# Kernel optimization log

Measured on AMD Instinct MI355X. Metric: run time of the kernel, lower is better.

The kernel has to match this reference:

```python
import jax, jax.numpy as jnp
import numpy as np

N_NODES = 50000
N_EDGES = 800000
IN_CH = 256
OUT_CH = 64  # heads=1
NEG_SLOPE = 0.2


def setup_inputs() -> dict:
    key = jax.random.key(0)
    k1, k2, k3, k4, k5 = jax.random.split(key, 5)
    x = jax.random.normal(k1, (N_NODES, IN_CH), dtype=jnp.float32)
    edge_index = jax.random.randint(k2, (2, N_EDGES), 0, N_NODES, dtype=jnp.int64)
    # glorot init for dense weight [out, in] (torch Linear layout) and att [out, 2]
    s_w = np.sqrt(6.0 / (OUT_CH + IN_CH)).astype(np.float32)
    W = jax.random.uniform(k3, (OUT_CH, IN_CH), minval=-s_w, maxval=s_w, dtype=jnp.float32)
    b = jnp.zeros((OUT_CH,), dtype=jnp.float32)
    s_a = np.sqrt(6.0 / (OUT_CH + 2)).astype(np.float32)
    att = jax.random.uniform(k4, (OUT_CH, 2), minval=-s_a, maxval=s_a, dtype=jnp.float32)
    return {"x": x, "edge_index": edge_index, "W": W, "b": b, "att": att}


def reference(x, edge_index, W, b, att):
    n = x.shape[0]
    # dense projection: feature [N, OUT_CH]
    feature = x @ W.T + b
    # per-node attention contributions: e_pre [N, 2]
    e_pre = feature @ att
    tar = edge_index[0]  # flow='target_to_source'
    src = edge_index[1]
    # edge logit = leakyrelu(a_tar(t) + a_src(s)); self-loop logit per node
    logit_edge = jax.nn.leaky_relu(e_pre[tar, 0] + e_pre[src, 1], NEG_SLOPE)
    logit_self = jax.nn.leaky_relu(e_pre[:, 0] + e_pre[:, 1], NEG_SLOPE)
    # segment softmax over {self edge} U {incoming edges} per target node
    m = jnp.maximum(jax.ops.segment_max(logit_edge, tar, num_segments=n), logit_self)
    exp_edge = jnp.exp(logit_edge - m[tar])
    exp_self = jnp.exp(logit_self - m)
    denom = exp_self + jax.ops.segment_sum(exp_edge, tar, num_segments=n)
    alpha = exp_edge / denom[tar]          # [E]
    alpha_self = exp_self / denom          # [N]
    # weighted gather-scatter aggregation (fused_gas_agg)
    msgs = alpha[:, None] * feature[src]   # [E, OUT_CH]
    out = alpha_self[:, None] * feature + jax.ops.segment_sum(msgs, tar, num_segments=n)
    return out
```

## Files before the change

### kernel.cpp

```cpp
#include <hip/hip_runtime.h>
#include <math.h>

#define N_NODES 50000
#define N_EDGES 800000
#define IN_CH 256
#define OUT_CH 64
#define NEG_SLOPE 0.2f

#define SCAN_BLK 256
#define N_SCAN_BLKS ((N_NODES + SCAN_BLK - 1) / SCAN_BLK)

typedef __bf16 bf16x4 __attribute__((ext_vector_type(4)));
typedef __bf16 bf16x8 __attribute__((ext_vector_type(8)));
typedef float  f32x4  __attribute__((ext_vector_type(4)));

__global__ __launch_bounds__(256) void k_gemm(
    const float* __restrict__ x, const float* __restrict__ W,
    const float* __restrict__ bias, const float* __restrict__ att,
    float* __restrict__ feature, float* __restrict__ e0,
    float* __restrict__ e1, int* __restrict__ deg)
{
    __shared__ __bf16 Ah[64][72];
    __shared__ __bf16 Al[64][72];
    __shared__ __bf16 Bh[64][72];
    __shared__ __bf16 Bl[64][72];

    const int t    = threadIdx.x;
    const int row0 = blockIdx.x * 64;
    const int wv   = t >> 6;
    const int li   = t & 63;
    const int lm   = li & 15;
    const int lq   = li >> 4;

    if (t < 64 && row0 + t < N_NODES) deg[row0 + t] = 0;

    f32x4 acc[4];
    #pragma unroll
    for (int tn = 0; tn < 4; ++tn) acc[tn] = (f32x4){0.f, 0.f, 0.f, 0.f};

    const int sr = t >> 2;
    const int cq = t & 3;

    for (int kc = 0; kc < IN_CH; kc += 64) {
        __syncthreads();
        {
            int gr = row0 + sr;
            #pragma unroll
            for (int i = 0; i < 4; ++i) {
                float4 v = make_float4(0.f, 0.f, 0.f, 0.f);
                if (gr < N_NODES)
                    v = *reinterpret_cast<const float4*>(&x[(size_t)gr * IN_CH + kc + cq * 16 + i * 4]);
                __bf16 hx = (__bf16)v.x, hy = (__bf16)v.y, hz = (__bf16)v.z, hw = (__bf16)v.w;
                bf16x4 h = {hx, hy, hz, hw};
                bf16x4 l = {(__bf16)(v.x - (float)hx), (__bf16)(v.y - (float)hy),
                            (__bf16)(v.z - (float)hz), (__bf16)(v.w - (float)hw)};
                *reinterpret_cast<bf16x4*>(&Ah[sr][cq * 16 + i * 4]) = h;
                *reinterpret_cast<bf16x4*>(&Al[sr][cq * 16 + i * 4]) = l;
            }
        }
        {
            #pragma unroll
            for (int i = 0; i < 4; ++i) {
                float4 v = *reinterpret_cast<const float4*>(&W[(size_t)sr * IN_CH + kc + cq * 16 + i * 4]);
                __bf16 hx = (__bf16)v.x, hy = (__bf16)v.y, hz = (__bf16)v.z, hw = (__bf16)v.w;
                bf16x4 h = {hx, hy, hz, hw};
                bf16x4 l = {(__bf16)(v.x - (float)hx), (__bf16)(v.y - (float)hy),
                            (__bf16)(v.z - (float)hz), (__bf16)(v.w - (float)hw)};
                *reinterpret_cast<bf16x4*>(&Bh[sr][cq * 16 + i * 4]) = h;
                *reinterpret_cast<bf16x4*>(&Bl[sr][cq * 16 + i * 4]) = l;
            }
        }
        __syncthreads();

        #pragma unroll
        for (int half = 0; half < 2; ++half) {
            int kb = half * 32 + lq * 8;
            bf16x8 ah = *reinterpret_cast<const bf16x8*>(&Ah[wv * 16 + lm][kb]);
            bf16x8 al = *reinterpret_cast<const bf16x8*>(&Al[wv * 16 + lm][kb]);
            #pragma unroll
            for (int tn = 0; tn < 4; ++tn) {
                bf16x8 bh = *reinterpret_cast<const bf16x8*>(&Bh[tn * 16 + lm][kb]);
                bf16x8 bl = *reinterpret_cast<const bf16x8*>(&Bl[tn * 16 + lm][kb]);
                acc[tn] = __builtin_amdgcn_mfma_f32_16x16x32_bf16(ah, bh, acc[tn], 0, 0, 0);
                acc[tn] = __builtin_amdgcn_mfma_f32_16x16x32_bf16(al, bh, acc[tn], 0, 0, 0);
                acc[tn] = __builtin_amdgcn_mfma_f32_16x16x32_bf16(ah, bl, acc[tn], 0, 0, 0);
            }
        }
    }

    float att0[4], att1[4], bv[4];
    #pragma unroll
    for (int tn = 0; tn < 4; ++tn) {
        int c = tn * 16 + lm;
        att0[tn] = att[c * 2 + 0];
        att1[tn] = att[c * 2 + 1];
        bv[tn]   = bias[c];
    }

    float p0[4] = {0.f, 0.f, 0.f, 0.f};
    float p1[4] = {0.f, 0.f, 0.f, 0.f};
    #pragma unroll
    for (int r = 0; r < 4; ++r) {
        int row = row0 + wv * 16 + lq * 4 + r;
        #pragma unroll
        for (int tn = 0; tn < 4; ++tn) {
            float f = acc[tn][r] + bv[tn];
            if (row < N_NODES)
                feature[(size_t)row * OUT_CH + tn * 16 + lm] = f;
            p0[r] += f * att0[tn];
            p1[r] += f * att1[tn];
        }
    }

    #pragma unroll
    for (int m = 1; m < 16; m <<= 1) {
        #pragma unroll
        for (int r = 0; r < 4; ++r) {
            p0[r] += __shfl_xor(p0[r], m, 64);
            p1[r] += __shfl_xor(p1[r], m, 64);
        }
    }
    if (lm == 0) {
        #pragma unroll
        for (int r = 0; r < 4; ++r) {
            int row = row0 + wv * 16 + lq * 4 + r;
            if (row < N_NODES) {
                e0[row] = p0[r];
                e1[row] = p1[r];
            }
        }
    }
}

__global__ __launch_bounds__(256) void k_hist(
    const int* __restrict__ ei, int* __restrict__ deg, int* __restrict__ e_slot)
{
    int e = blockIdx.x * blockDim.x + threadIdx.x;
    if (e >= N_EDGES) return;
    e_slot[e] = atomicAdd(&deg[ei[e]], 1);
}

__global__ __launch_bounds__(SCAN_BLK) void k_scan_blk(
    const int* __restrict__ deg, int* __restrict__ offl, int* __restrict__ bsum)
{
    __shared__ int s[SCAN_BLK];
    int tid = threadIdx.x;
    int i = blockIdx.x * SCAN_BLK + tid;
    int v = (i < N_NODES) ? deg[i] : 0;
    s[tid] = v;
    __syncthreads();
    #pragma unroll
    for (int d = 1; d < SCAN_BLK; d <<= 1) {
        int u = (tid >= d) ? s[tid - d] : 0;
        __syncthreads();
        s[tid] += u;
        __syncthreads();
    }
    if (i < N_NODES) offl[i] = s[tid] - v;
    if (tid == SCAN_BLK - 1) bsum[blockIdx.x] = s[tid];
}

__global__ __launch_bounds__(256) void k_scan_top(
    const int* __restrict__ bsum, int* __restrict__ boff)
{
    __shared__ int s[256];
    int tid = threadIdx.x;
    int v = (tid < N_SCAN_BLKS) ? bsum[tid] : 0;
    s[tid] = v;
    __syncthreads();
    #pragma unroll
    for (int d = 1; d < 256; d <<= 1) {
        int u = (tid >= d) ? s[tid - d] : 0;
        __syncthreads();
        s[tid] += u;
        __syncthreads();
    }
    if (tid < N_SCAN_BLKS) boff[tid] = s[tid] - v;
    if (tid == 0) boff[N_SCAN_BLKS] = N_EDGES;
}

__global__ __launch_bounds__(256) void k_fill(
    const int* __restrict__ ei, const int* __restrict__ offl,
    const int* __restrict__ boff, const int* __restrict__ e_slot,
    int* __restrict__ csr)
{
    int e = blockIdx.x * blockDim.x + threadIdx.x;
    if (e >= N_EDGES) return;
    int tnode = ei[e];
    int snode = ei[N_EDGES + e];
    csr[offl[tnode] + boff[tnode >> 8] + e_slot[e]] = snode;
}

__global__ __launch_bounds__(256) void k_gather(
    const float* __restrict__ e0, const float* __restrict__ e1,
    const float* __restrict__ feature, const int* __restrict__ offl,
    const int* __restrict__ boff, const int* __restrict__ csr,
    float* __restrict__ out)
{
    int t = blockIdx.x * 4 + (threadIdx.x >> 6);
    int c = threadIdx.x & 63;
    if (t >= N_NODES) return;

    float e0t = e0[t];
    float z   = e0t + e1[t];
    float lr  = z > 0.f ? z : NEG_SLOPE * z;
    float wsf = expf(lr);

    float acc  = wsf * feature[(size_t)t * OUT_CH + c];
    float wsum = wsf;

    int e   = offl[t] + boff[t >> 8];
    int end = (t + 1 < N_NODES) ? (offl[t + 1] + boff[(t + 1) >> 8]) : N_EDGES;

    for (; e + 4 <= end; e += 4) {
        int s0 = csr[e], s1 = csr[e + 1], s2 = csr[e + 2], s3 = csr[e + 3];
        float q0 = e1[s0], q1 = e1[s1], q2 = e1[s2], q3 = e1[s3];
        float f0 = feature[(size_t)s0 * OUT_CH + c];
        float f1 = feature[(size_t)s1 * OUT_CH + c];
        float f2 = feature[(size_t)s2 * OUT_CH + c];
        float f3 = feature[(size_t)s3 * OUT_CH + c];
        float z0 = e0t + q0, z1 = e0t + q1, z2 = e0t + q2, z3 = e0t + q3;
        float w0 = expf(z0 > 0.f ? z0 : NEG_SLOPE * z0);
        float w1 = expf(z1 > 0.f ? z1 : NEG_SLOPE * z1);
        float w2 = expf(z2 > 0.f ? z2 : NEG_SLOPE * z2);
        float w3 = expf(z3 > 0.f ? z3 : NEG_SLOPE * z3);
        acc += w0 * f0 + w1 * f1 + w2 * f2 + w3 * f3;
        wsum += (w0 + w1) + (w2 + w3);
    }
    for (; e < end; ++e) {
        int s0 = csr[e];
        float q0 = e1[s0];
        float f0 = feature[(size_t)s0 * OUT_CH + c];
        float z0 = e0t + q0;
        float w0 = expf(z0 > 0.f ? z0 : NEG_SLOPE * z0);
        acc += w0 * f0;
        wsum += w0;
    }
    out[(size_t)t * OUT_CH + c] = acc / wsum;
}

extern "C" void kernel_launch(void* const* d_in, const int* in_sizes, int n_in,
                              void* d_out, int out_size, void* d_ws, size_t ws_size,
                              hipStream_t stream)
{
    const float* x    = (const float*)d_in[0];
    const int*   ei   = (const int*)d_in[1];
    const float* W    = (const float*)d_in[2];
    const float* bias = (const float*)d_in[3];
    const float* att  = (const float*)d_in[4];
    float* out = (float*)d_out;

    float* ws      = (float*)d_ws;
    float* feature = ws;
    float* e0      = feature + (size_t)N_NODES * OUT_CH;
    float* e1      = e0 + N_NODES;
    int*   csr     = (int*)(e1 + N_NODES);
    int*   deg     = csr + N_EDGES;
    int*   offl    = deg + N_NODES;
    int*   bsum    = offl + N_NODES;
    int*   boff    = bsum + N_SCAN_BLKS;
    int*   e_slot  = boff + N_SCAN_BLKS + 1;

    dim3 blk(256);

    k_gemm<<<dim3((N_NODES + 63) / 64), blk, 0, stream>>>(
        x, W, bias, att, feature, e0, e1, deg);

    k_hist<<<dim3((N_EDGES + 255) / 256), blk, 0, stream>>>(ei, deg, e_slot);

    k_scan_blk<<<dim3(N_SCAN_BLKS), dim3(SCAN_BLK), 0, stream>>>(deg, offl, bsum);
    k_scan_top<<<dim3(1), dim3(256), 0, stream>>>(bsum, boff);

    k_fill<<<dim3((N_EDGES + 255) / 256), blk, 0, stream>>>(
        ei, offl, boff, e_slot, csr);

    k_gather<<<dim3((N_NODES + 3) / 4), blk, 0, stream>>>(
        e0, e1, feature, offl, boff, csr, out);
}
```

Baseline: 199.2 us.

## Store features in bf16, drop split-bf16 GEMM correction, use fast exp

The projection GEMM stops emulating fp32 with hi/lo bf16 splits and runs a single bf16 MFMA pass. The full K=256 tile is now staged in shared memory once instead of being looped over K chunks. The intermediate feature matrix is written and gathered as bf16, which halves the bytes of the random per-edge feature gathers. Exp calls become __expf. Accuracy drops, since features and GEMM inputs are rounded to bf16, and the larger LDS footprint may lower occupancy.

```diff
diff --git a/kernel.cpp b/kernel.cpp
--- a/kernel.cpp
+++ b/kernel.cpp
@@ -17,13 +17,11 @@
 __global__ __launch_bounds__(256) void k_gemm(
     const float* __restrict__ x, const float* __restrict__ W,
     const float* __restrict__ bias, const float* __restrict__ att,
-    float* __restrict__ feature, float* __restrict__ e0,
+    __bf16* __restrict__ featb, float* __restrict__ e0,
     float* __restrict__ e1, int* __restrict__ deg)
 {
-    __shared__ __bf16 Ah[64][72];
-    __shared__ __bf16 Al[64][72];
-    __shared__ __bf16 Bh[64][72];
-    __shared__ __bf16 Bl[64][72];
+    __shared__ __bf16 A[64][264];
+    __shared__ __bf16 B[64][264];
 
     const int t    = threadIdx.x;
     const int row0 = blockIdx.x * 64;
@@ -34,57 +32,42 @@
 
     if (t < 64 && row0 + t < N_NODES) deg[row0 + t] = 0;
 
-    f32x4 acc[4];
-    #pragma unroll
-    for (int tn = 0; tn < 4; ++tn) acc[tn] = (f32x4){0.f, 0.f, 0.f, 0.f};
-
     const int sr = t >> 2;
     const int cq = t & 3;
-
-    for (int kc = 0; kc < IN_CH; kc += 64) {
-        __syncthreads();
-        {
-            int gr = row0 + sr;
+    {
+        int gr = row0 + sr;
+        bool ok = (gr < N_NODES);
+        #pragma unroll
+        for (int j = 0; j < 4; ++j) {
             #pragma unroll
             for (int i = 0; i < 4; ++i) {
+                int kk = j * 64 + cq * 16 + i * 4;
                 float4 v = make_float4(0.f, 0.f, 0.f, 0.f);
-                if (gr < N_NODES)
-                    v = *reinterpret_cast<const float4*>(&x[(size_t)gr * IN_CH + kc + cq * 16 + i * 4]);
-                __bf16 hx = (__bf16)v.x, hy = (__bf16)v.y, hz = (__bf16)v.z, hw = (__bf16)v.w;
-                bf16x4 h = {hx, hy, hz, hw};
-                bf16x4 l = {(__bf16)(v.x - (float)hx), (__bf16)(v.y - (float)hy),
-                            (__bf16)(v.z - (float)hz), (__bf16)(v.w - (float)hw)};
-                *reinterpret_cast<bf16x4*>(&Ah[sr][cq * 16 + i * 4]) = h;
-                *reinterpret_cast<bf16x4*>(&Al[sr][cq * 16 + i * 4]) = l;
+                if (ok)
+                    v = *reinterpret_cast<const float4*>(&x[(size_t)gr * IN_CH + kk]);
+                bf16x4 h = {(__bf16)v.x, (__bf16)v.y, (__bf16)v.z, (__bf16)v.w};
+                *reinterpret_cast<bf16x4*>(&A[sr][kk]) = h;
+
+                float4 w1 = *reinterpret_cast<const float4*>(&W[(size_t)sr * IN_CH + kk]);
+                bf16x4 g = {(__bf16)w1.x, (__bf16)w1.y, (__bf16)w1.z, (__bf16)w1.w};
+                *reinterpret_cast<bf16x4*>(&B[sr][kk]) = g;
             }
         }
-        {
-            #pragma unroll
-            for (int i = 0; i < 4; ++i) {
-                float4 v = *reinterpret_cast<const float4*>(&W[(size_t)sr * IN_CH + kc + cq * 16 + i * 4]);
-                __bf16 hx = (__bf16)v.x, hy = (__bf16)v.y, hz = (__bf16)v.z, hw = (__bf16)v.w;
-                bf16x4 h = {hx, hy, hz, hw};
-                bf16x4 l = {(__bf16)(v.x - (float)hx), (__bf16)(v.y - (float)hy),
-                            (__bf16)(v.z - (float)hz), (__bf16)(v.w - (float)hw)};
-                *reinterpret_cast<bf16x4*>(&Bh[sr][cq * 16 + i * 4]) = h;
-                *reinterpret_cast<bf16x4*>(&Bl[sr][cq * 16 + i * 4]) = l;
-            }
-        }
-        __syncthreads();
-
-        #pragma unroll
-        for (int half = 0; half < 2; ++half) {
-            int kb = half * 32 + lq * 8;
-            bf16x8 ah = *reinterpret_cast<const bf16x8*>(&Ah[wv * 16 + lm][kb]);
-            bf16x8 al = *reinterpret_cast<const bf16x8*>(&Al[wv * 16 + lm][kb]);
-            #pragma unroll
-            for (int tn = 0; tn < 4; ++tn) {
-                bf16x8 bh = *reinterpret_cast<const bf16x8*>(&Bh[tn * 16 + lm][kb]);
-                bf16x8 bl = *reinterpret_cast<const bf16x8*>(&Bl[tn * 16 + lm][kb]);
-                acc[tn] = __builtin_amdgcn_mfma_f32_16x16x32_bf16(ah, bh, acc[tn], 0, 0, 0);
-                acc[tn] = __builtin_amdgcn_mfma_f32_16x16x32_bf16(al, bh, acc[tn], 0, 0, 0);
-                acc[tn] = __builtin_amdgcn_mfma_f32_16x16x32_bf16(ah, bl, acc[tn], 0, 0, 0);
-            }
+    }
+    __syncthreads();
+
+    f32x4 acc[4];
+    #pragma unroll
+    for (int tn = 0; tn < 4; ++tn) acc[tn] = (f32x4){0.f, 0.f, 0.f, 0.f};
+
+    #pragma unroll
+    for (int kb = 0; kb < 8; ++kb) {
+        int ko = kb * 32 + lq * 8;
+        bf16x8 a = *reinterpret_cast<const bf16x8*>(&A[wv * 16 + lm][ko]);
+        #pragma unroll
+        for (int tn = 0; tn < 4; ++tn) {
+            bf16x8 b = *reinterpret_cast<const bf16x8*>(&B[tn * 16 + lm][ko]);
+            acc[tn] = __builtin_amdgcn_mfma_f32_16x16x32_bf16(a, b, acc[tn], 0, 0, 0);
         }
     }
 
@@ -106,7 +89,7 @@
         for (int tn = 0; tn < 4; ++tn) {
             float f = acc[tn][r] + bv[tn];
             if (row < N_NODES)
-                feature[(size_t)row * OUT_CH + tn * 16 + lm] = f;
+                featb[(size_t)row * OUT_CH + tn * 16 + lm] = (__bf16)f;
             p0[r] += f * att0[tn];
             p1[r] += f * att1[tn];
         }
@@ -193,7 +176,7 @@
 
 __global__ __launch_bounds__(256) void k_gather(
     const float* __restrict__ e0, const float* __restrict__ e1,
-    const float* __restrict__ feature, const int* __restrict__ offl,
+    const __bf16* __restrict__ featb, const int* __restrict__ offl,
     const int* __restrict__ boff, const int* __restrict__ csr,
     float* __restrict__ out)
 {
@@ -204,9 +187,9 @@
     float e0t = e0[t];
     float z   = e0t + e1[t];
     float lr  = z > 0.f ? z : NEG_SLOPE * z;
-    float wsf = expf(lr);
-
-    float acc  = wsf * feature[(size_t)t * OUT_CH + c];
+    float wsf = __expf(lr);
+
+    float acc  = wsf * (float)featb[(size_t)t * OUT_CH + c];
     float wsum = wsf;
 
     int e   = offl[t] + boff[t >> 8];
@@ -215,24 +198,24 @@
     for (; e + 4 <= end; e += 4) {
         int s0 = csr[e], s1 = csr[e + 1], s2 = csr[e + 2], s3 = csr[e + 3];
         float q0 = e1[s0], q1 = e1[s1], q2 = e1[s2], q3 = e1[s3];
-        float f0 = feature[(size_t)s0 * OUT_CH + c];
-        float f1 = feature[(size_t)s1 * OUT_CH + c];
-        float f2 = feature[(size_t)s2 * OUT_CH + c];
-        float f3 = feature[(size_t)s3 * OUT_CH + c];
+        float f0 = (float)featb[(size_t)s0 * OUT_CH + c];
+        float f1 = (float)featb[(size_t)s1 * OUT_CH + c];
+        float f2 = (float)featb[(size_t)s2 * OUT_CH + c];
+        float f3 = (float)featb[(size_t)s3 * OUT_CH + c];
         float z0 = e0t + q0, z1 = e0t + q1, z2 = e0t + q2, z3 = e0t + q3;
-        float w0 = expf(z0 > 0.f ? z0 : NEG_SLOPE * z0);
-        float w1 = expf(z1 > 0.f ? z1 : NEG_SLOPE * z1);
-        float w2 = expf(z2 > 0.f ? z2 : NEG_SLOPE * z2);
-        float w3 = expf(z3 > 0.f ? z3 : NEG_SLOPE * z3);
+        float w0 = __expf(z0 > 0.f ? z0 : NEG_SLOPE * z0);
+        float w1 = __expf(z1 > 0.f ? z1 : NEG_SLOPE * z1);
+        float w2 = __expf(z2 > 0.f ? z2 : NEG_SLOPE * z2);
+        float w3 = __expf(z3 > 0.f ? z3 : NEG_SLOPE * z3);
         acc += w0 * f0 + w1 * f1 + w2 * f2 + w3 * f3;
         wsum += (w0 + w1) + (w2 + w3);
     }
     for (; e < end; ++e) {
         int s0 = csr[e];
         float q0 = e1[s0];
-        float f0 = feature[(size_t)s0 * OUT_CH + c];
+        float f0 = (float)featb[(size_t)s0 * OUT_CH + c];
         float z0 = e0t + q0;
-        float w0 = expf(z0 > 0.f ? z0 : NEG_SLOPE * z0);
+        float w0 = __expf(z0 > 0.f ? z0 : NEG_SLOPE * z0);
         acc += w0 * f0;
         wsum += w0;
     }
@@ -250,21 +233,20 @@
     const float* att  = (const float*)d_in[4];
     float* out = (float*)d_out;
 
-    float* ws      = (float*)d_ws;
-    float* feature = ws;
-    float* e0      = feature + (size_t)N_NODES * OUT_CH;
-    float* e1      = e0 + N_NODES;
-    int*   csr     = (int*)(e1 + N_NODES);
-    int*   deg     = csr + N_EDGES;
-    int*   offl    = deg + N_NODES;
-    int*   bsum    = offl + N_NODES;
-    int*   boff    = bsum + N_SCAN_BLKS;
-    int*   e_slot  = boff + N_SCAN_BLKS + 1;
+    __bf16* featb = (__bf16*)d_ws;
+    float*  e0    = (float*)(featb + (size_t)N_NODES * OUT_CH);
+    float*  e1    = e0 + N_NODES;
+    int*    csr   = (int*)(e1 + N_NODES);
+    int*    deg   = csr + N_EDGES;
+    int*    offl  = deg + N_NODES;
+    int*    bsum  = offl + N_NODES;
+    int*    boff  = bsum + N_SCAN_BLKS;
+    int*    e_slot= boff + N_SCAN_BLKS + 1;
 
     dim3 blk(256);
 
     k_gemm<<<dim3((N_NODES + 63) / 64), blk, 0, stream>>>(
-        x, W, bias, att, feature, e0, e1, deg);
+        x, W, bias, att, featb, e0, e1, deg);
 
     k_hist<<<dim3((N_EDGES + 255) / 256), blk, 0, stream>>>(ei, deg, e_slot);
 
@@ -275,5 +257,5 @@
         ei, offl, boff, e_slot, csr);
 
     k_gather<<<dim3((N_NODES + 3) / 4), blk, 0, stream>>>(
-        e0, e1, feature, offl, boff, csr, out);
-}
+        e0, e1, featb, offl, boff, csr, out);
+}
```

New measurement: 197.9 us. No clear change (-0.6%).
